# Kernel optimization log

Measured on AMD Instinct MI355X. Metric: run time of the kernel, lower is better.

Reference implementation:

```python
import jax, jax.numpy as jnp
import numpy as np

EMBED_DIM = 256
NUM_HEADS = 4
HEAD_DIM = EMBED_DIM // NUM_HEADS
SCALE = HEAD_DIM ** (-0.5)


def setup_inputs() -> dict:
    key = jax.random.key(0)
    kx, kq, kp, kb = jax.random.split(key, 4)
    B, N, C = 4, 4096, EMBED_DIM
    x = jax.random.normal(kx, (B, N, C), dtype=jnp.float32)
    # qkv: Linear(C, 3C, bias=False); torch stores weight as [out, in]
    w_qkv = jax.random.normal(kq, (3 * C, C), dtype=jnp.float32) * (C ** -0.5)
    w_proj = jax.random.normal(kp, (C, C), dtype=jnp.float32) * (C ** -0.5)
    b_proj = jax.random.normal(kb, (C,), dtype=jnp.float32) * 0.01
    return {"x": x, "w_qkv": w_qkv, "w_proj": w_proj, "b_proj": b_proj}


def reference(x, w_qkv, w_proj, b_proj):
    B, N, C = x.shape
    H, D = NUM_HEADS, HEAD_DIM
    # qkv projection: [B,N,3C] -> [3,B,H,N,D]
    qkv = (x @ w_qkv.T).reshape(B, N, 3, H, D).transpose(2, 0, 3, 1, 4)
    q, k, v = qkv[0], qkv[1], qkv[2]
    # materialized [B,H,N,N] scores (faithful to the original)
    attn = jnp.einsum("bhnd,bhmd->bhnm", q, k) * SCALE
    attn_probs = jax.nn.softmax(attn, axis=-1)
    out = jnp.einsum("bhnm,bhmd->bhnd", attn_probs, v)
    out = out.transpose(0, 2, 1, 3).reshape(B, N, C)
    return out @ w_proj.T + b_proj
```

## Files before the change

### kernel.cpp

```cpp
#include <hip/hip_runtime.h>
#include <hip/hip_bf16.h>

typedef __hip_bfloat16 bf16;
typedef _Float16 f16;
typedef __attribute__((ext_vector_type(8))) short bf16x8;
typedef __attribute__((ext_vector_type(8))) _Float16 f16x8;
typedef __attribute__((ext_vector_type(2))) _Float16 f16x2;
typedef __attribute__((ext_vector_type(4))) float f32x4;
typedef __attribute__((ext_vector_type(4))) unsigned int u32x4;
typedef __attribute__((ext_vector_type(2))) unsigned int u32x2;

#define B_ 4
#define N_ 4096
#define C_ 256
#define H_ 4
#define D_ 64
#define KLN 0.18033688011112042f

#if __has_builtin(__builtin_amdgcn_exp2f)
#define EXP2(x) __builtin_amdgcn_exp2f(x)
#else
#define EXP2(x) exp2f(x)
#endif
#if __has_builtin(__builtin_amdgcn_rcpf)
#define RCP(x) __builtin_amdgcn_rcpf(x)
#else
#define RCP(x) (1.0f / (x))
#endif

__device__ inline void load_lds16(const void* g, void* l) {
#if __has_builtin(__builtin_amdgcn_global_load_lds)
    __builtin_amdgcn_global_load_lds(
        (const __attribute__((address_space(1))) unsigned int*)g,
        (__attribute__((address_space(3))) unsigned int*)l, 16, 0, 0);
#else
    int ln = __lane_id();
    ((u32x4*)l)[ln] = *((const u32x4*)g);
#endif
}

__device__ inline unsigned int pk2(float a, float b) {
    unsigned int ua = __builtin_bit_cast(unsigned int, a) + 0x8000u;
    unsigned int ub = __builtin_bit_cast(unsigned int, b) + 0x8000u;
    return (ua >> 16) | (ub & 0xffff0000u);
}
__device__ inline unsigned int pkh2(float a, float b) {
#if __has_builtin(__builtin_amdgcn_cvt_pkrtz)
    return __builtin_bit_cast(unsigned int, __builtin_amdgcn_cvt_pkrtz(a, b));
#else
    f16x2 h = { (f16)a, (f16)b };
    return __builtin_bit_cast(unsigned int, h);
#endif
}

__global__ __launch_bounds__(256) void cast_bf16(const float* __restrict__ x,
                                                 const float* __restrict__ wq,
                                                 const float* __restrict__ wp,
                                                 bf16* __restrict__ xb,
                                                 bf16* __restrict__ wqb,
                                                 bf16* __restrict__ wpb)
{
    int bid = blockIdx.x;
    const float* s; bf16* d; int base;
    if (bid < 2048)      { s = x;  d = xb;  base = bid * 2048; }
    else if (bid < 2144) { s = wq; d = wqb; base = (bid - 2048) * 2048; }
    else                 { s = wp; d = wpb; base = (bid - 2144) * 2048; }
    int i = base + threadIdx.x * 8;
    f32x4 a = *reinterpret_cast<const f32x4*>(s + i);
    f32x4 b = *reinterpret_cast<const f32x4*>(s + i + 4);
    u32x4 o;
    o.x = pk2(a[0], a[1]); o.y = pk2(a[2], a[3]);
    o.z = pk2(b[0], b[1]); o.w = pk2(b[2], b[3]);
    *reinterpret_cast<u32x4*>(d + i) = o;
}

__global__ __launch_bounds__(256, 2) void qkv_fast(const bf16* __restrict__ x,
                                                   const bf16* __restrict__ w,
                                                   bf16* __restrict__ qw,
                                                   bf16* __restrict__ kw,
                                                   f16* __restrict__ vtw)
{
    __shared__ short w_s[64][264];
    const int tid  = threadIdx.x;
    const int lane = tid & 63;
    const int wav  = tid >> 6;
    const int quad = lane >> 4;
    const int l16  = lane & 15;
    const int bid = (blockIdx.x & 7) * 192 + (blockIdx.x >> 3);
    const int mt = bid / 12, nb = bid % 12;
    const int m0 = mt * 128, n0 = nb * 64;

    {
        const int row = tid >> 2, cb = (tid & 3) * 64;
        const bf16* src = w + (size_t)(n0 + row) * C_ + cb;
#pragma unroll
        for (int i = 0; i < 8; ++i)
            *reinterpret_cast<bf16x8*>(&w_s[row][cb + i * 8]) =
                *reinterpret_cast<const bf16x8*>(src + i * 8);
    }
    __syncthreads();

#pragma unroll
    for (int half = 0; half < 2; ++half) {
        const int mh = m0 + half * 64;
        f32x4 acc[4] = {{0,0,0,0},{0,0,0,0},{0,0,0,0},{0,0,0,0}};
        const bf16* xrow = x + (size_t)(mh + wav * 16 + l16) * C_ + quad * 8;
        if (nb < 8) {
#pragma unroll
            for (int k0 = 0; k0 < C_; k0 += 32) {
                bf16x8 a = *reinterpret_cast<const bf16x8*>(xrow + k0);
#pragma unroll
                for (int nt = 0; nt < 4; ++nt) {
                    bf16x8 b = *reinterpret_cast<const bf16x8*>(&w_s[nt * 16 + l16][k0 + quad * 8]);
                    acc[nt] = __builtin_amdgcn_mfma_f32_16x16x32_bf16(b, a, acc[nt], 0, 0, 0);
                }
            }
        } else {
#pragma unroll
            for (int k0 = 0; k0 < C_; k0 += 32) {
                bf16x8 a = *reinterpret_cast<const bf16x8*>(xrow + k0);
#pragma unroll
                for (int nt = 0; nt < 4; ++nt) {
                    bf16x8 b = *reinterpret_cast<const bf16x8*>(&w_s[nt * 16 + l16][k0 + quad * 8]);
                    acc[nt] = __builtin_amdgcn_mfma_f32_16x16x32_bf16(a, b, acc[nt], 0, 0, 0);
                }
            }
        }

        const int bb = mh >> 12;
        const int nbase = (mh + wav * 16) & (N_ - 1);
        if (nb < 4) {
            bf16* dst = qw + (((size_t)bb * H_ + nb) * N_ + nbase + l16) * D_;
#pragma unroll
            for (int nt = 0; nt < 4; ++nt) {
                u32x2 wv = { pk2(acc[nt][0] * KLN, acc[nt][1] * KLN),
                             pk2(acc[nt][2] * KLN, acc[nt][3] * KLN) };
                *reinterpret_cast<u32x2*>(dst + nt * 16 + quad * 4) = wv;
            }
        } else if (nb < 8) {
            bf16* dst = kw + (((size_t)bb * H_ + (nb - 4)) * N_ + nbase + l16) * D_;
#pragma unroll
            for (int nt = 0; nt < 4; ++nt) {
                u32x2 wv = { pk2(acc[nt][0], acc[nt][1]),
                             pk2(acc[nt][2], acc[nt][3]) };
                *reinterpret_cast<u32x2*>(dst + nt * 16 + quad * 4) = wv;
            }
        } else {
            const int h = nb - 8;
#pragma unroll
            for (int nt = 0; nt < 4; ++nt) {
                int d = nt * 16 + l16;
                u32x2 wv;
                wv.x = pkh2(acc[nt][0], acc[nt][1]);
                wv.y = pkh2(acc[nt][2], acc[nt][3]);
                *reinterpret_cast<u32x2*>(
                    vtw + (((size_t)bb * H_ + h) * D_ + d) * N_ + nbase + quad * 4) = wv;
            }
        }
    }
}

__global__ __launch_bounds__(256, 2) void attn(const bf16* __restrict__ q,
                                               const bf16* __restrict__ k,
                                               const f16* __restrict__ vt,
                                               bf16* __restrict__ o)
{
    __shared__ __align__(16) char smem[40960];
    short* k_s = reinterpret_cast<short*>(smem);
    f16*   v_s = reinterpret_cast<f16*>(smem + 16384);

    const int tid  = threadIdx.x;
    const int lane = tid & 63;
    const int wav  = tid >> 6;
    const int quad = lane >> 4;
    const int l16  = lane & 15;
    const int l8   = lane & 7;

    const int wg = (blockIdx.x & 7) * 64 + (blockIdx.x >> 3);
    const int bh = wg >> 5;
    const int qt = wg & 31;
    const int bb = bh >> 2, h = bh & 3;

    const bf16* qp = q  + (size_t)bh * N_ * D_;
    const bf16* kp = k  + (size_t)bh * N_ * D_;
    const f16*  vp = vt + (size_t)bh * D_ * N_;

    const int qbase = qt * 128 + wav * 32;
    bf16x8 qb[2][2];
#pragma unroll
    for (int qg = 0; qg < 2; ++qg)
#pragma unroll
        for (int ks = 0; ks < 2; ++ks)
            qb[qg][ks] = *reinterpret_cast<const bf16x8*>(
                qp + (size_t)(qbase + qg * 16 + l16) * D_ + ks * 32 + quad * 8);

    const int ri = lane >> 3;
    const int ci = lane & 7;
    const int gc = ci ^ ri;
    int koff[2], voff[2], lds_r[2];
#pragma unroll
    for (int g = 0; g < 2; ++g) {
        const int rb  = wav * 16 + g * 8;
        const int rho = rb + ri;
        const int pr  = (rho & 32) | ((rho & 12) << 1) | ((rho & 16) >> 2) | (rho & 3);
        koff[g]  = pr * D_ + gc * 8;
        voff[g]  = rho * N_ + gc * 8;
        lds_r[g] = rb * 64;
    }

    f32x4 oacc[2][4];
    f32x4 lacc[2];
#pragma unroll
    for (int qg = 0; qg < 2; ++qg) {
        lacc[qg] = (f32x4){0, 0, 0, 0};
#pragma unroll
        for (int dt = 0; dt < 4; ++dt) oacc[qg][dt] = (f32x4){0, 0, 0, 0};
    }
    const f16x8 onesA = {1.f16, 1.f16, 1.f16, 1.f16, 1.f16, 1.f16, 1.f16, 1.f16};

    f32x4 s[2][4];
    f16x8 pbE[2][2], pbO[2][2];

#define STAGE(kbuf, vslot, t) do {                                            \
    const int j0_ = (t) * 64;                                                 \
    short* kd_ = k_s + (kbuf) * 4096;                                         \
    f16*   vd_ = v_s + (vslot) * 4096;                                        \
    load_lds16(kp + (size_t)j0_ * D_ + koff[0], kd_ + lds_r[0]);              \
    load_lds16(kp + (size_t)j0_ * D_ + koff[1], kd_ + lds_r[1]);              \
    load_lds16(vp + j0_ + voff[0],              vd_ + lds_r[0]);              \
    load_lds16(vp + j0_ + voff[1],              vd_ + lds_r[1]);              \
} while (0)

#define QK(kbuf) do {                                                         \
    const short* kt_ = k_s + (kbuf) * 4096;                                   \
    _Pragma("unroll")                                                         \
    for (int nt = 0; nt < 4; ++nt) {                                          \
        const int rb_ = (nt * 16 + l16) * 64;                                 \
        bf16x8 ka0_ = *reinterpret_cast<const bf16x8*>(kt_ + rb_ + ((quad    ) ^ l8) * 8); \
        bf16x8 ka1_ = *reinterpret_cast<const bf16x8*>(kt_ + rb_ + ((4 + quad) ^ l8) * 8); \
        _Pragma("unroll")                                                     \
        for (int qg = 0; qg < 2; ++qg) {                                      \
            s[qg][nt] = __builtin_amdgcn_mfma_f32_16x16x32_bf16(              \
                ka0_, qb[qg][0], (f32x4){0.f, 0.f, 0.f, 0.f}, 0, 0, 0);       \
            s[qg][nt] = __builtin_amdgcn_mfma_f32_16x16x32_bf16(              \
                ka1_, qb[qg][1], s[qg][nt], 0, 0, 0);                         \
        }                                                                     \
    }                                                                         \
} while (0)

#define PV(vslot, PB) do {                                                    \
    const f16* vt_ = v_s + (vslot) * 4096;                                    \
    lacc[0] = __builtin_amdgcn_mfma_f32_16x16x32_f16(onesA, PB[0][0], lacc[0], 0, 0, 0); \
    lacc[0] = __builtin_amdgcn_mfma_f32_16x16x32_f16(onesA, PB[0][1], lacc[0], 0, 0, 0); \
    lacc[1] = __builtin_amdgcn_mfma_f32_16x16x32_f16(onesA, PB[1][0], lacc[1], 0, 0, 0); \
    lacc[1] = __builtin_amdgcn_mfma_f32_16x16x32_f16(onesA, PB[1][1], lacc[1], 0, 0, 0); \
    _Pragma("unroll")                                                         \
    for (int ks = 0; ks < 2; ++ks) {                                          \
        _Pragma("unroll")                                                     \
        for (int dt = 0; dt < 4; ++dt) {                                      \
            f16x8 va_ = *reinterpret_cast<const f16x8*>(                      \
                vt_ + (dt * 16 + l16) * 64 + (((ks << 2) + quad) ^ l8) * 8);  \
            oacc[0][dt] = __builtin_amdgcn_mfma_f32_16x16x32_f16(va_, PB[0][ks], oacc[0][dt], 0, 0, 0); \
            oacc[1][dt] = __builtin_amdgcn_mfma_f32_16x16x32_f16(va_, PB[1][ks], oacc[1][dt], 0, 0, 0); \
        }                                                                     \
    }                                                                         \
} while (0)

#define EXPP(PB) do {                                                         \
    _Pragma("unroll")                                                         \
    for (int qg = 0; qg < 2; ++qg) {                                          \
        _Pragma("unroll")                                                     \
        for (int ks = 0; ks < 2; ++ks) {                                      \
            const f32x4 sa_ = s[qg][2 * ks], sb_ = s[qg][2 * ks + 1];         \
            u32x4 pw_;                                                        \
            pw_.x = pkh2(EXP2(sa_[0]), EXP2(sa_[1]));                         \
            pw_.y = pkh2(EXP2(sa_[2]), EXP2(sa_[3]));                         \
            pw_.z = pkh2(EXP2(sb_[0]), EXP2(sb_[1]));                         \
            pw_.w = pkh2(EXP2(sb_[2]), EXP2(sb_[3]));                         \
            PB[qg][ks] = __builtin_bit_cast(f16x8, pw_);                      \
        }                                                                     \
    }                                                                         \
} while (0)

#define SB __builtin_amdgcn_sched_barrier(0)

    STAGE(0, 0, 0);
    __syncthreads();

    STAGE(1, 1, 1);
    QK(0); EXPP(pbE);
    __syncthreads();

    STAGE(0, 2, 2);
    PV(0, pbE); SB; QK(1); EXPP(pbO);
    __syncthreads();

#pragma unroll 1
    for (int tb = 2; tb <= 56; tb += 6) {
        STAGE(1, 0, tb + 1);
        PV(1, pbO); SB; QK(0); EXPP(pbE);
        __syncthreads();
        STAGE(0, 1, tb + 2);
        PV(2, pbE); SB; QK(1); EXPP(pbO);
        __syncthreads();
        STAGE(1, 2, tb + 3);
        PV(0, pbO); SB; QK(0); EXPP(pbE);
        __syncthreads();
        STAGE(0, 0, tb + 4);
        PV(1, pbE); SB; QK(1); EXPP(pbO);
        __syncthreads();
        STAGE(1, 1, tb + 5);
        PV(2, pbO); SB; QK(0); EXPP(pbE);
        __syncthreads();
        STAGE(0, 2, tb + 6);
        PV(0, pbE); SB; QK(1); EXPP(pbO);
        __syncthreads();
    }
    STAGE(1, 0, 63);
    PV(1, pbO); SB; QK(0); EXPP(pbE);
    __syncthreads();
    PV(2, pbE); SB; QK(1); EXPP(pbO);
    PV(0, pbO);

#pragma unroll
    for (int qg = 0; qg < 2; ++qg) {
        const float rl = RCP(lacc[qg][0]);
        const size_t obase = ((size_t)bb * N_ + qbase + qg * 16 + l16) * C_ + h * D_;
#pragma unroll
        for (int dt = 0; dt < 4; ++dt) {
            float v0 = oacc[qg][dt][0] * rl;
            float v1 = oacc[qg][dt][1] * rl;
            float v2 = oacc[qg][dt][2] * rl;
            float v3 = oacc[qg][dt][3] * rl;
            u32x2 wv = { pk2(v0, v1), pk2(v2, v3) };
            *reinterpret_cast<u32x2*>(o + obase + dt * 16 + quad * 4) = wv;
        }
    }
}

__global__ __launch_bounds__(256, 2) void out_proj_fast(const bf16* __restrict__ ov,
                                                        const bf16* __restrict__ w,
                                                        const float* __restrict__ bias,
                                                        float* __restrict__ out)
{
    __shared__ short w_s[64][264];
    const int tid  = threadIdx.x;
    const int lane = tid & 63;
    const int wav  = tid >> 6;
    const int quad = lane >> 4;
    const int l16  = lane & 15;
    const int bid = (blockIdx.x & 7) * 64 + (blockIdx.x >> 3);
    const int m0 = (bid >> 2) * 128;
    const int n0 = (bid & 3) * 64;

    {
        const int row = tid >> 2, cb = (tid & 3) * 64;
        const bf16* src = w + (size_t)(n0 + row) * C_ + cb;
#pragma unroll
        for (int i = 0; i < 8; ++i)
            *reinterpret_cast<bf16x8*>(&w_s[row][cb + i * 8]) =
                *reinterpret_cast<const bf16x8*>(src + i * 8);
    }
    __syncthreads();

#pragma unroll
    for (int half = 0; half < 2; ++half) {
        const int mh = m0 + half * 64;
        f32x4 acc[4] = {{0,0,0,0},{0,0,0,0},{0,0,0,0},{0,0,0,0}};
        const bf16* orow = ov + (size_t)(mh + wav * 16 + l16) * C_ + quad * 8;
#pragma unroll
        for (int k0 = 0; k0 < C_; k0 += 32) {
            bf16x8 a = *reinterpret_cast<const bf16x8*>(orow + k0);
#pragma unroll
            for (int nt = 0; nt < 4; ++nt) {
                bf16x8 b = *reinterpret_cast<const bf16x8*>(&w_s[nt * 16 + l16][k0 + quad * 8]);
                acc[nt] = __builtin_amdgcn_mfma_f32_16x16x32_bf16(b, a, acc[nt], 0, 0, 0);
            }
        }
        const int m = mh + wav * 16 + l16;
#pragma unroll
        for (int nt = 0; nt < 4; ++nt) {
            const int oc0 = n0 + nt * 16 + quad * 4;
            f32x4 bv = *reinterpret_cast<const f32x4*>(bias + oc0);
            f32x4 ovv = acc[nt] + bv;
            *reinterpret_cast<f32x4*>(out + (size_t)m * C_ + oc0) = ovv;
        }
    }
}

extern "C" void kernel_launch(void* const* d_in, const int* in_sizes, int n_in,
                              void* d_out, int out_size, void* d_ws, size_t ws_size,
                              hipStream_t stream) {
    const float* x      = (const float*)d_in[0];
    const float* w_qkv  = (const float*)d_in[1];
    const float* w_proj = (const float*)d_in[2];
    const float* b_proj = (const float*)d_in[3];
    float* out = (float*)d_out;

    const size_t qkv_elems = (size_t)B_ * H_ * N_ * D_;
    bf16* q_ws  = (bf16*)d_ws;
    bf16* k_ws  = q_ws  + qkv_elems;
    f16*  vt_ws = (f16*)(k_ws + qkv_elems);
    bf16* o_ws  = (bf16*)(vt_ws + qkv_elems);
    bf16* x_bf  = o_ws  + qkv_elems;
    bf16* wq_bf = x_bf  + (size_t)B_ * N_ * C_;
    bf16* wp_bf = wq_bf + (size_t)3 * C_ * C_;

    cast_bf16    <<<2176, 256, 0, stream>>>(x, w_qkv, w_proj, x_bf, wq_bf, wp_bf);
    qkv_fast     <<<1536, 256, 0, stream>>>(x_bf, wq_bf, q_ws, k_ws, vt_ws);
    attn         <<< 512, 256, 0, stream>>>(q_ws, k_ws, vt_ws, o_ws);
    out_proj_fast<<< 512, 256, 0, stream>>>(o_ws, wp_bf, b_proj, out);
}
```

Measured before the change: 174.3 us.

## Halve per-wave query rows in attention to double grid and occupancy

Each wave now handles 16 query rows instead of 32, so a workgroup covers 64 queries. The grid doubles to 1024 blocks and launch bounds ask for 4 blocks per CU instead of 2. This cuts accumulator registers and adds parallelism to hide latency. The cost is that every K/V tile staged into LDS is reused by half as many queries, which doubles global and LDS traffic for K and V.

```diff
diff --git a/kernel.cpp b/kernel.cpp
--- a/kernel.cpp
+++ b/kernel.cpp
@@ -160,7 +160,7 @@
     }
 }
 
-__global__ __launch_bounds__(256, 2) void attn(const bf16* __restrict__ q,
+__global__ __launch_bounds__(256, 4) void attn(const bf16* __restrict__ q,
                                                const bf16* __restrict__ k,
                                                const f16* __restrict__ vt,
                                                bf16* __restrict__ o)
@@ -176,23 +176,21 @@
     const int l16  = lane & 15;
     const int l8   = lane & 7;
 
-    const int wg = (blockIdx.x & 7) * 64 + (blockIdx.x >> 3);
-    const int bh = wg >> 5;
-    const int qt = wg & 31;
+    const int wg = (blockIdx.x & 7) * 128 + (blockIdx.x >> 3);
+    const int bh = wg >> 6;
+    const int qt = wg & 63;
     const int bb = bh >> 2, h = bh & 3;
 
     const bf16* qp = q  + (size_t)bh * N_ * D_;
     const bf16* kp = k  + (size_t)bh * N_ * D_;
     const f16*  vp = vt + (size_t)bh * D_ * N_;
 
-    const int qbase = qt * 128 + wav * 32;
-    bf16x8 qb[2][2];
-#pragma unroll
-    for (int qg = 0; qg < 2; ++qg)
-#pragma unroll
-        for (int ks = 0; ks < 2; ++ks)
-            qb[qg][ks] = *reinterpret_cast<const bf16x8*>(
-                qp + (size_t)(qbase + qg * 16 + l16) * D_ + ks * 32 + quad * 8);
+    const int qbase = qt * 64 + wav * 16;
+    bf16x8 qb0, qb1;
+    qb0 = *reinterpret_cast<const bf16x8*>(
+        qp + (size_t)(qbase + l16) * D_ + quad * 8);
+    qb1 = *reinterpret_cast<const bf16x8*>(
+        qp + (size_t)(qbase + l16) * D_ + 32 + quad * 8);
 
     const int ri = lane >> 3;
     const int ci = lane & 7;
@@ -208,18 +206,14 @@
         lds_r[g] = rb * 64;
     }
 
-    f32x4 oacc[2][4];
-    f32x4 lacc[2];
-#pragma unroll
-    for (int qg = 0; qg < 2; ++qg) {
-        lacc[qg] = (f32x4){0, 0, 0, 0};
-#pragma unroll
-        for (int dt = 0; dt < 4; ++dt) oacc[qg][dt] = (f32x4){0, 0, 0, 0};
-    }
+    f32x4 oacc[4];
+    f32x4 lacc = (f32x4){0, 0, 0, 0};
+#pragma unroll
+    for (int dt = 0; dt < 4; ++dt) oacc[dt] = (f32x4){0, 0, 0, 0};
     const f16x8 onesA = {1.f16, 1.f16, 1.f16, 1.f16, 1.f16, 1.f16, 1.f16, 1.f16};
 
-    f32x4 s[2][4];
-    f16x8 pbE[2][2], pbO[2][2];
+    f32x4 s[4];
+    f16x8 pbE[2], pbO[2];
 
 #define STAGE(kbuf, vslot, t) do {                                            \
     const int j0_ = (t) * 64;                                                 \
@@ -238,47 +232,38 @@
         const int rb_ = (nt * 16 + l16) * 64;                                 \
         bf16x8 ka0_ = *reinterpret_cast<const bf16x8*>(kt_ + rb_ + ((quad    ) ^ l8) * 8); \
         bf16x8 ka1_ = *reinterpret_cast<const bf16x8*>(kt_ + rb_ + ((4 + quad) ^ l8) * 8); \
-        _Pragma("unroll")                                                     \
-        for (int qg = 0; qg < 2; ++qg) {                                      \
-            s[qg][nt] = __builtin_amdgcn_mfma_f32_16x16x32_bf16(              \
-                ka0_, qb[qg][0], (f32x4){0.f, 0.f, 0.f, 0.f}, 0, 0, 0);       \
-            s[qg][nt] = __builtin_amdgcn_mfma_f32_16x16x32_bf16(              \
-                ka1_, qb[qg][1], s[qg][nt], 0, 0, 0);                         \
-        }                                                                     \
+        s[nt] = __builtin_amdgcn_mfma_f32_16x16x32_bf16(                      \
+            ka0_, qb0, (f32x4){0.f, 0.f, 0.f, 0.f}, 0, 0, 0);                 \
+        s[nt] = __builtin_amdgcn_mfma_f32_16x16x32_bf16(                      \
+            ka1_, qb1, s[nt], 0, 0, 0);                                       \
     }                                                                         \
 } while (0)
 
 #define PV(vslot, PB) do {                                                    \
     const f16* vt_ = v_s + (vslot) * 4096;                                    \
-    lacc[0] = __builtin_amdgcn_mfma_f32_16x16x32_f16(onesA, PB[0][0], lacc[0], 0, 0, 0); \
-    lacc[0] = __builtin_amdgcn_mfma_f32_16x16x32_f16(onesA, PB[0][1], lacc[0], 0, 0, 0); \
-    lacc[1] = __builtin_amdgcn_mfma_f32_16x16x32_f16(onesA, PB[1][0], lacc[1], 0, 0, 0); \
-    lacc[1] = __builtin_amdgcn_mfma_f32_16x16x32_f16(onesA, PB[1][1], lacc[1], 0, 0, 0); \
+    lacc = __builtin_amdgcn_mfma_f32_16x16x32_f16(onesA, PB[0], lacc, 0, 0, 0); \
+    lacc = __builtin_amdgcn_mfma_f32_16x16x32_f16(onesA, PB[1], lacc, 0, 0, 0); \
     _Pragma("unroll")                                                         \
     for (int ks = 0; ks < 2; ++ks) {                                          \
         _Pragma("unroll")                                                     \
         for (int dt = 0; dt < 4; ++dt) {                                      \
             f16x8 va_ = *reinterpret_cast<const f16x8*>(                      \
                 vt_ + (dt * 16 + l16) * 64 + (((ks << 2) + quad) ^ l8) * 8);  \
-            oacc[0][dt] = __builtin_amdgcn_mfma_f32_16x16x32_f16(va_, PB[0][ks], oacc[0][dt], 0, 0, 0); \
-            oacc[1][dt] = __builtin_amdgcn_mfma_f32_16x16x32_f16(va_, PB[1][ks], oacc[1][dt], 0, 0, 0); \
+            oacc[dt] = __builtin_amdgcn_mfma_f32_16x16x32_f16(va_, PB[ks], oacc[dt], 0, 0, 0); \
         }                                                                     \
     }                                                                         \
 } while (0)
 
 #define EXPP(PB) do {                                                         \
     _Pragma("unroll")                                                         \
-    for (int qg = 0; qg < 2; ++qg) {                                          \
-        _Pragma("unroll")                                                     \
-        for (int ks = 0; ks < 2; ++ks) {                                      \
-            const f32x4 sa_ = s[qg][2 * ks], sb_ = s[qg][2 * ks + 1];         \
-            u32x4 pw_;                                                        \
-            pw_.x = pkh2(EXP2(sa_[0]), EXP2(sa_[1]));                         \
-            pw_.y = pkh2(EXP2(sa_[2]), EXP2(sa_[3]));                         \
-            pw_.z = pkh2(EXP2(sb_[0]), EXP2(sb_[1]));                         \
-            pw_.w = pkh2(EXP2(sb_[2]), EXP2(sb_[3]));                         \
-            PB[qg][ks] = __builtin_bit_cast(f16x8, pw_);                      \
-        }                                                                     \
+    for (int ks = 0; ks < 2; ++ks) {                                          \
+        const f32x4 sa_ = s[2 * ks], sb_ = s[2 * ks + 1];                     \
+        u32x4 pw_;                                                            \
+        pw_.x = pkh2(EXP2(sa_[0]), EXP2(sa_[1]));                             \
+        pw_.y = pkh2(EXP2(sa_[2]), EXP2(sa_[3]));                             \
+        pw_.z = pkh2(EXP2(sb_[0]), EXP2(sb_[1]));                             \
+        pw_.w = pkh2(EXP2(sb_[2]), EXP2(sb_[3]));                             \
+        PB[ks] = __builtin_bit_cast(f16x8, pw_);                              \
     }                                                                         \
 } while (0)
 
@@ -322,16 +307,15 @@
     PV(2, pbE); SB; QK(1); EXPP(pbO);
     PV(0, pbO);
 
-#pragma unroll
-    for (int qg = 0; qg < 2; ++qg) {
-        const float rl = RCP(lacc[qg][0]);
-        const size_t obase = ((size_t)bb * N_ + qbase + qg * 16 + l16) * C_ + h * D_;
+    {
+        const float rl = RCP(lacc[0]);
+        const size_t obase = ((size_t)bb * N_ + qbase + l16) * C_ + h * D_;
 #pragma unroll
         for (int dt = 0; dt < 4; ++dt) {
-            float v0 = oacc[qg][dt][0] * rl;
-            float v1 = oacc[qg][dt][1] * rl;
-            float v2 = oacc[qg][dt][2] * rl;
-            float v3 = oacc[qg][dt][3] * rl;
+            float v0 = oacc[dt][0] * rl;
+            float v1 = oacc[dt][1] * rl;
+            float v2 = oacc[dt][2] * rl;
+            float v3 = oacc[dt][3] * rl;
             u32x2 wv = { pk2(v0, v1), pk2(v2, v3) };
             *reinterpret_cast<u32x2*>(o + obase + dt * 16 + quad * 4) = wv;
         }
@@ -408,6 +392,6 @@
 
     cast_bf16    <<<2176, 256, 0, stream>>>(x, w_qkv, w_proj, x_bf, wq_bf, wp_bf);
     qkv_fast     <<<1536, 256, 0, stream>>>(x_bf, wq_bf, q_ws, k_ws, vt_ws);
-    attn         <<< 512, 256, 0, stream>>>(q_ws, k_ws, vt_ws, o_ws);
+    attn         <<<1024, 256, 0, stream>>>(q_ws, k_ws, vt_ws, o_ws);
     out_proj_fast<<< 512, 256, 0, stream>>>(o_ws, wp_bf, b_proj, out);
 }
```

Result: slower. 188.4 us (+8.1%).
